# Kernel optimization log

Hardware: AMD Instinct MI355X
Metric: run time of the kernel (lower is better)

## Reference

```python
import jax, jax.numpy as jnp
import numpy as np

B, L, C, OUT = 32, 1024, 64, 64
BN_EPS = 1e-5  # PyTorch BatchNorm1d default


def setup_inputs() -> dict:
    key = jax.random.key(0)
    kH, kA, kW = jax.random.split(key, 3)
    H = jax.random.normal(kH, (B, L, C), dtype=jnp.float32)
    A = jax.random.uniform(kA, (B, L, L), dtype=jnp.float32)  # positive degrees
    gamma = jnp.ones((C,), jnp.float32)
    beta = jnp.zeros((C,), jnp.float32)
    W = jax.random.normal(kW, (C, OUT), dtype=jnp.float32) * 0.05
    b = jnp.zeros((OUT,), jnp.float32)
    return {"H": H, "A": A, "gamma": gamma, "beta": beta, "W": W, "b": b}


def reference(H, A, gamma, beta, W, b):
    batch, l, c = H.shape
    # BatchNorm1d in train mode over the flattened (batch*l, c) node axis,
    # biased variance as in PyTorch.
    Hf = H.reshape(batch * l, c)
    mean = Hf.mean(axis=0)
    var = jnp.mean((Hf - mean) ** 2, axis=0)
    Hn = ((Hf - mean) * jax.lax.rsqrt(var + BN_EPS) * gamma + beta).reshape(batch, l, c)
    # Degree normalization: diag(d^0.5) @ A @ diag(d^-0.5) done as row/col scaling
    # (same math as the original's dense diagonal matmuls).
    d = A.sum(axis=2)                                   # [batch, l]
    A_norm = jnp.sqrt(d)[:, :, None] * A * jax.lax.rsqrt(d)[:, None, :]
    A_hat = jnp.eye(l, dtype=A.dtype) - A_norm          # I - D^0.5 A D^-0.5
    # Linear then batched propagation, LeakyReLU (default slope 0.01).
    X = Hn @ W + b                                      # [batch, l, out]
    out = jnp.einsum('bij,bjo->bio', A_hat, X)
    return jax.nn.leaky_relu(out, negative_slope=0.01)
```

## Files before the change

kernel.cpp:

```cpp
#include <hip/hip_runtime.h>

#define NB 32
#define NL 1024
#define NC 64
#define NO 64
constexpr float BN_EPS = 1e-5f;

#define D_OFF 128
#define PART_OFF 32896
#define YT_OFF 131072

typedef short          s16x8 __attribute__((ext_vector_type(8)));
typedef float          f32x16 __attribute__((ext_vector_type(16)));
typedef float          f32x4  __attribute__((ext_vector_type(4)));

__device__ inline unsigned short f2bf(float f) {
    union { float f; unsigned u; } v; v.f = f;
    unsigned u = v.u + 0x7FFFu + ((v.u >> 16) & 1u);
    return (unsigned short)(u >> 16);
}

__device__ inline void gload16(const void* g, void* l) {
    __builtin_amdgcn_global_load_lds(
        (const __attribute__((address_space(1))) unsigned int*)g,
        (__attribute__((address_space(3))) unsigned int*)l, 16, 0, 0);
}

__device__ inline s16x8 cvt8(f32x4 lo, f32x4 hi) {
    union { unsigned int i[4]; s16x8 v; } u;
    asm("v_cvt_pk_bf16_f32 %0, %1, %2" : "=v"(u.i[0]) : "v"(lo.x), "v"(lo.y));
    asm("v_cvt_pk_bf16_f32 %0, %1, %2" : "=v"(u.i[1]) : "v"(lo.z), "v"(lo.w));
    asm("v_cvt_pk_bf16_f32 %0, %1, %2" : "=v"(u.i[2]) : "v"(hi.x), "v"(hi.y));
    asm("v_cvt_pk_bf16_f32 %0, %1, %2" : "=v"(u.i[3]) : "v"(hi.z), "v"(hi.w));
    return u.v;
}

__global__ __launch_bounds__(256) void deg_bn(
    const float* __restrict__ A, const float* __restrict__ H,
    float* __restrict__ ws) {
    __shared__ f32x4 smem4[3072];
    const int t = threadIdx.x;
    if (blockIdx.x < 1024) {
        const int lane = t & 63, w = t >> 6;
        const size_t row0 = (size_t)blockIdx.x * 32;
        const char* src = (const char*)A + row0 * 4096;
        const int lo = w * 4096 + lane * 16;
#define STG(bi, c) do {                                                        \
            char* d0 = (char*)smem4 + (bi) * 16384 + lo;                       \
            const char* s0 = src + (c) * 16384 + lo;                           \
            gload16(s0,        d0);                                            \
            gload16(s0 + 1024, d0 + 1024);                                     \
            gload16(s0 + 2048, d0 + 2048);                                     \
            gload16(s0 + 3072, d0 + 3072);                                     \
        } while (0)
        STG(0, 0); STG(1, 1); STG(2, 2);
        int cb = 0;
#pragma unroll 1
        for (int c = 0; c < 8; ++c) {
            if (c <= 5)      asm volatile("s_waitcnt vmcnt(8)" ::: "memory");
            else if (c == 6) asm volatile("s_waitcnt vmcnt(4)" ::: "memory");
            else             asm volatile("s_waitcnt vmcnt(0)" ::: "memory");
            __builtin_amdgcn_sched_barrier(0);
            const char* cbp = (const char*)smem4 + cb * 16384 + lo;
            float s = 0.f;
#pragma unroll
            for (int j = 0; j < 4; ++j) {
                f32x4 v = *(const f32x4*)(cbp + j * 1024);
                s += v.x + v.y + v.z + v.w;
            }
#pragma unroll
            for (int m = 32; m; m >>= 1) s += __shfl_xor(s, m, 64);
            if (lane == 0) ws[D_OFF + row0 + c * 4 + w] = s;
            __builtin_amdgcn_sched_barrier(0);
            if (c + 3 < 8) STG(cb, c + 3);
            cb = (cb == 2) ? 0 : cb + 1;
        }
#undef STG
    } else {
        const int bb = blockIdx.x - 1024;
        const float4* Hv = (const float4*)H + bb * 4096;
        float s0 = 0.f, s1 = 0.f, s2 = 0.f, s3 = 0.f;
        float q0 = 0.f, q1 = 0.f, q2 = 0.f, q3 = 0.f;
#pragma unroll 4
        for (int s = 0; s < 16; ++s) {
            float4 v = Hv[s * 256 + t];
            s0 += v.x; q0 += v.x * v.x;
            s1 += v.y; q1 += v.y * v.y;
            s2 += v.z; q2 += v.z * v.z;
            s3 += v.w; q3 += v.w * v.w;
        }
        float* part = (float*)smem4;
        part[t * 8 + 0] = s0; part[t * 8 + 1] = s1;
        part[t * 8 + 2] = s2; part[t * 8 + 3] = s3;
        part[t * 8 + 4] = q0; part[t * 8 + 5] = q1;
        part[t * 8 + 6] = q2; part[t * 8 + 7] = q3;
        __syncthreads();
        if (t < 64) {
            const int g = t >> 2, e = t & 3;
            float a = 0.f, a2 = 0.f;
#pragma unroll
            for (int k = 0; k < 16; ++k) {
                a  += part[(g + 16 * k) * 8 + e];
                a2 += part[(g + 16 * k) * 8 + 4 + e];
            }
            ws[PART_OFF + bb * 64 + t] = a;
            ws[PART_OFF + 128 * 64 + bb * 64 + t] = a2;
        }
    }
}

__global__ __launch_bounds__(256) void linear_xy(
    const float* __restrict__ H, const float* __restrict__ Wm,
    const float* __restrict__ bias, const float* __restrict__ gamma,
    const float* __restrict__ beta, const float* __restrict__ ws,
    float* __restrict__ X, unsigned short* __restrict__ Yt) {
    __shared__ float Wl[NC * NO];
    __shared__ float hnbuf[4][NC];
    __shared__ unsigned short ytile[64][66];
    __shared__ float ls[256], ls2[256];
    __shared__ float sscale[64], sshift[64];
    const int b = blockIdx.x >> 4, ch = blockIdx.x & 15;
    const int r0g = b * NL + ch * 64;
    const int t = threadIdx.x, lane = t & 63, w = t >> 6;
    {
        const float* ps  = ws + PART_OFF;
        const float* ps2 = ws + PART_OFF + 128 * 64;
        const int c = t & 63, q = t >> 6;
        float s = 0.f, s2 = 0.f;
        for (int p = q * 32; p < q * 32 + 32; ++p) {
            s  += ps[p * 64 + c];
            s2 += ps2[p * 64 + c];
        }
        ls[t] = s; ls2[t] = s2;
        __syncthreads();
        if (t < 64) {
            float T  = ls[c]  + ls[c + 64]  + ls[c + 128]  + ls[c + 192];
            float T2 = ls2[c] + ls2[c + 64] + ls2[c + 128] + ls2[c + 192];
            const float n = (float)(NB * NL);
            float mean = T / n;
            float var  = T2 / n - mean * mean;
            float sc = gamma[c] * rsqrtf(var + BN_EPS);
            sscale[c] = sc;
            sshift[c] = beta[c] - mean * sc;
        }
    }
    for (int k = t; k < NC * NO; k += 256) Wl[k] = Wm[k];
    __syncthreads();
    const float sc = sscale[lane];
    const float sh = sshift[lane];
    const float bo = bias[lane];
    const float* dbuf = ws + D_OFF;
    for (int rr = w; rr < 64; rr += 4) {
        const int row = r0g + rr;
        float h = H[(size_t)row * NC + lane];
        hnbuf[w][lane] = h * sc + sh;
        float x = bo;
#pragma unroll
        for (int c4 = 0; c4 < NC; c4 += 4) {
            float4 h4 = *(const float4*)(&hnbuf[w][c4]);
            x += h4.x * Wl[(c4 + 0) * NO + lane];
            x += h4.y * Wl[(c4 + 1) * NO + lane];
            x += h4.z * Wl[(c4 + 2) * NO + lane];
            x += h4.w * Wl[(c4 + 3) * NO + lane];
        }
        X[(size_t)row * NO + lane] = x;
        ytile[rr][lane] = f2bf(x * rsqrtf(dbuf[row]));
    }
    __syncthreads();
    char* ybase = (char*)Yt + (size_t)(b * 16 + ch) * 8192;
#pragma unroll
    for (int i2 = 0; i2 < 16; ++i2) {
        const int col = i2 * 4 + w;
        *(unsigned short*)(ybase + ((col * 128 + lane * 2) ^ ((col & 7) << 4))) =
            ytile[lane][col];
    }
}

__global__ __launch_bounds__(256) void prop_mfma(
    const float* __restrict__ A, const unsigned short* __restrict__ Yt,
    const float* __restrict__ dbuf, float* __restrict__ XO) {

    __shared__ float Abuf[2][64 * 64];
    __shared__ unsigned short Ybuf[2][64 * 64];
    __shared__ float sdl[64];

    const int b  = blockIdx.x >> 4;
    const int mt = blockIdx.x & 15;
    const int i0 = mt * 64;
    const char* Abase = (const char*)A + ((size_t)(b * NL + i0)) * 4096;
    const char* YbT   = (const char*)Yt + (size_t)b * 16 * 8192;

    const int t    = threadIdx.x;
    const int lane = t & 63;
    const int w    = t >> 6;

    if (t < 64) sdl[t] = sqrtf(dbuf[b * NL + i0 + t]);

    const int tr = t >> 4;
    const int tc = (t & 15) * 16;
    const char* As[4];
#pragma unroll
    for (int i = 0; i < 4; ++i) {
        const int row = i * 16 + tr;
        As[i] = Abase + (size_t)row * 4096 + (tc ^ ((row & 7) << 4));
    }
    const int yL0 = t * 16, yL1 = t * 16 + 4096;

    const int wr0  = (w >> 1) * 32;
    const int wc0  = (w & 1) * 32;
    const int frow = wr0 + (lane & 31);
    const int fcol = wc0 + (lane & 31);
    const int khb  = (lane >> 5) * 16;
    const int kfh  = (lane >> 5) * 32;
    const int swA  = (frow & 7) << 4;
    const int swY  = (fcol & 7) << 4;

    f32x16 acc;
#pragma unroll
    for (int r = 0; r < 16; ++r) acc[r] = 0.f;

#define STAGE(bi, kt) do {                                                     \
        char* ad = (char*)Abuf[bi];                                            \
        gload16(As[0] + (kt) * 256, ad + t * 16);                              \
        gload16(As[1] + (kt) * 256, ad + 4096  + t * 16);                      \
        gload16(As[2] + (kt) * 256, ad + 8192  + t * 16);                      \
        gload16(As[3] + (kt) * 256, ad + 12288 + t * 16);                      \
        const char* ys = YbT + (size_t)(kt) * 8192;                            \
        char* yd = (char*)Ybuf[bi];                                            \
        gload16(ys + yL0, yd + yL0);                                           \
        gload16(ys + yL1, yd + yL1);                                           \
    } while (0)

    STAGE(0, 0);
    __syncthreads();

#pragma unroll 1
    for (int kti = 0; kti < 16; ++kti) {
        const int nxt = kti + 1;
        if (nxt < 16) STAGE(nxt & 1, nxt);
        const char* ab  = (const char*)Abuf[kti & 1];
        const char* yb2 = (const char*)Ybuf[kti & 1];
#pragma unroll
        for (int ks = 0; ks < 4; ++ks) {
            const int b0 = frow * 256 + ks * 64 + kfh;
            f32x4 flo = *(const f32x4*)(ab + ((b0)      ^ swA));
            f32x4 fhi = *(const f32x4*)(ab + ((b0 + 16) ^ swA));
            s16x8 af = cvt8(flo, fhi);
            s16x8 bf = *(const s16x8*)(yb2 + ((fcol * 128 + ks * 32 + khb) ^ swY));
            acc = __builtin_amdgcn_mfma_f32_32x32x16_bf16(af, bf, acc, 0, 0, 0);
        }
        __syncthreads();
    }
#undef STAGE

#pragma unroll
    for (int reg = 0; reg < 16; ++reg) {
        int row = (reg & 3) + 8 * (reg >> 2) + 4 * (lane >> 5);
        int i   = i0 + wr0 + row;
        int col = wc0 + (lane & 31);
        size_t idx = ((size_t)(b * NL + i)) * NO + col;
        float x = XO[idx];
        float v = x - sdl[wr0 + row] * acc[reg];
        XO[idx] = v > 0.f ? v : 0.01f * v;
    }
}

extern "C" void kernel_launch(void* const* d_in, const int* in_sizes, int n_in,
                              void* d_out, int out_size, void* d_ws, size_t ws_size,
                              hipStream_t stream) {
    const float* H     = (const float*)d_in[0];
    const float* A     = (const float*)d_in[1];
    const float* gamma = (const float*)d_in[2];
    const float* beta  = (const float*)d_in[3];
    const float* Wm    = (const float*)d_in[4];
    const float* bias  = (const float*)d_in[5];
    float* out = (float*)d_out;
    float* ws  = (float*)d_ws;
    unsigned short* Yt = (unsigned short*)(ws + YT_OFF);

    deg_bn<<<1152, 256, 0, stream>>>(A, H, ws);
    linear_xy<<<512, 256, 0, stream>>>(H, Wm, bias, gamma, beta, ws, out, Yt);
    prop_mfma<<<512, 256, 0, stream>>>(A, Yt, ws + D_OFF, out);
}
```

Measured before the change: 69.95 us.

## Compute linear layer with bf16 MFMA and fold batchnorm into weights

Replaces the per-row scalar FMA loop in linear_xy with a 32x32x16 bf16 MFMA tile product. The H tile is loaded asynchronously into swizzled LDS, and the batchnorm scale is folded into a bf16 copy of W while the shift is folded into the bias. This targets the scalar LDS-bound matmul cost of the linear stage. In exchange X now goes through bf16 inputs, which lowers precision, and the kernel uses more shared memory.

New measurement: 61.10 us, median of 2. -12.6%, faster.

```diff
diff --git a/kernel.cpp b/kernel.cpp
--- a/kernel.cpp
+++ b/kernel.cpp
@@ -114,14 +114,33 @@
     const float* __restrict__ bias, const float* __restrict__ gamma,
     const float* __restrict__ beta, const float* __restrict__ ws,
     float* __restrict__ X, unsigned short* __restrict__ Yt) {
-    __shared__ float Wl[NC * NO];
-    __shared__ float hnbuf[4][NC];
+    __shared__ float Hl[64 * 64];
+    __shared__ float Wl[64 * 64];
+    __shared__ unsigned short Wbf[64 * 64];
     __shared__ unsigned short ytile[64][66];
     __shared__ float ls[256], ls2[256];
-    __shared__ float sscale[64], sshift[64];
+    __shared__ float sscale[64], sshift[64], bp[64], sdl[64];
     const int b = blockIdx.x >> 4, ch = blockIdx.x & 15;
     const int r0g = b * NL + ch * 64;
     const int t = threadIdx.x, lane = t & 63, w = t >> 6;
+
+    {
+        const char* hsrc = (const char*)H + (size_t)r0g * 256;
+#pragma unroll
+        for (int i = 0; i < 4; ++i) {
+            const int L = i * 4096 + t * 16;
+            const int row = L >> 8, cb = L & 255;
+            gload16(hsrc + (size_t)row * 256 + (cb ^ ((row & 7) << 4)),
+                    (char*)Hl + L);
+        }
+    }
+    {
+        const float4* Wv = (const float4*)Wm;
+        float4* Wd = (float4*)Wl;
+#pragma unroll
+        for (int k = 0; k < 4; ++k) Wd[t + k * 256] = Wv[t + k * 256];
+    }
+    if (t < 64) sdl[t] = rsqrtf(ws[D_OFF + r0g + t]);
     {
         const float* ps  = ws + PART_OFF;
         const float* ps2 = ws + PART_OFF + 128 * 64;
@@ -132,39 +151,69 @@
             s2 += ps2[p * 64 + c];
         }
         ls[t] = s; ls2[t] = s2;
-        __syncthreads();
-        if (t < 64) {
-            float T  = ls[c]  + ls[c + 64]  + ls[c + 128]  + ls[c + 192];
-            float T2 = ls2[c] + ls2[c + 64] + ls2[c + 128] + ls2[c + 192];
-            const float n = (float)(NB * NL);
-            float mean = T / n;
-            float var  = T2 / n - mean * mean;
-            float sc = gamma[c] * rsqrtf(var + BN_EPS);
-            sscale[c] = sc;
-            sshift[c] = beta[c] - mean * sc;
-        }
-    }
-    for (int k = t; k < NC * NO; k += 256) Wl[k] = Wm[k];
-    __syncthreads();
-    const float sc = sscale[lane];
-    const float sh = sshift[lane];
-    const float bo = bias[lane];
-    const float* dbuf = ws + D_OFF;
-    for (int rr = w; rr < 64; rr += 4) {
-        const int row = r0g + rr;
-        float h = H[(size_t)row * NC + lane];
-        hnbuf[w][lane] = h * sc + sh;
-        float x = bo;
-#pragma unroll
-        for (int c4 = 0; c4 < NC; c4 += 4) {
-            float4 h4 = *(const float4*)(&hnbuf[w][c4]);
-            x += h4.x * Wl[(c4 + 0) * NO + lane];
-            x += h4.y * Wl[(c4 + 1) * NO + lane];
-            x += h4.z * Wl[(c4 + 2) * NO + lane];
-            x += h4.w * Wl[(c4 + 3) * NO + lane];
-        }
-        X[(size_t)row * NO + lane] = x;
-        ytile[rr][lane] = f2bf(x * rsqrtf(dbuf[row]));
+    }
+    __syncthreads();
+    if (t < 64) {
+        const int c = t;
+        float T  = ls[c]  + ls[c + 64]  + ls[c + 128]  + ls[c + 192];
+        float T2 = ls2[c] + ls2[c + 64] + ls2[c + 128] + ls2[c + 192];
+        const float n = (float)(NB * NL);
+        float mean = T / n;
+        float var  = T2 / n - mean * mean;
+        float sc = gamma[c] * rsqrtf(var + BN_EPS);
+        sscale[c] = sc;
+        sshift[c] = beta[c] - mean * sc;
+    }
+    __syncthreads();
+    {
+        float p = 0.f;
+#pragma unroll
+        for (int c0 = 0; c0 < 16; ++c0) {
+            const int c = w * 16 + c0;
+            p += sshift[c] * Wl[c * 64 + lane];
+        }
+        ls[t] = p;
+    }
+#pragma unroll
+    for (int c0 = 0; c0 < 16; ++c0) {
+        const int c = w * 16 + c0;
+        const float v = sscale[c] * Wl[c * 64 + lane];
+        *(unsigned short*)((char*)Wbf + ((lane * 128 + c * 2) ^ ((lane & 7) << 4)))
+            = f2bf(v);
+    }
+    __syncthreads();
+    if (t < 64) bp[t] = bias[t] + ls[t] + ls[t + 64] + ls[t + 128] + ls[t + 192];
+    __syncthreads();
+
+    const int wr0  = (w >> 1) * 32;
+    const int wc0  = (w & 1) * 32;
+    const int frow = wr0 + (lane & 31);
+    const int fcol = wc0 + (lane & 31);
+    const int khb  = (lane >> 5) * 16;
+    const int kfh  = (lane >> 5) * 32;
+    const int swA  = (frow & 7) << 4;
+    const int swY  = (fcol & 7) << 4;
+    f32x16 acc;
+#pragma unroll
+    for (int r = 0; r < 16; ++r) acc[r] = 0.f;
+    const char* ab = (const char*)Hl;
+    const char* wb = (const char*)Wbf;
+#pragma unroll
+    for (int ks = 0; ks < 4; ++ks) {
+        const int b0 = frow * 256 + ks * 64 + kfh;
+        f32x4 flo = *(const f32x4*)(ab + ((b0)      ^ swA));
+        f32x4 fhi = *(const f32x4*)(ab + ((b0 + 16) ^ swA));
+        s16x8 af = cvt8(flo, fhi);
+        s16x8 bf = *(const s16x8*)(wb + ((fcol * 128 + ks * 32 + khb) ^ swY));
+        acc = __builtin_amdgcn_mfma_f32_32x32x16_bf16(af, bf, acc, 0, 0, 0);
+    }
+#pragma unroll
+    for (int reg = 0; reg < 16; ++reg) {
+        const int row = wr0 + (reg & 3) + 8 * (reg >> 2) + 4 * (lane >> 5);
+        const int col = wc0 + (lane & 31);
+        const float x = acc[reg] + bp[col];
+        X[(size_t)(r0g + row) * NO + col] = x;
+        ytile[row][col] = f2bf(x * sdl[row]);
     }
     __syncthreads();
     char* ybase = (char*)Yt + (size_t)(b * 16 + ch) * 8192;
```
